# Performance work log

Measured on AMD Instinct MI355X. Metric: run time of the kernel, lower is better.

## Reference

```python
import jax, jax.numpy as jnp
import numpy as np

B = 8192        # number of contexts
T_SIDE = 10     # num_cx_tokens_per_side
NT = 10         # cx_max_num_types
V_TOK = 5000
V_TYP = 5000
D_TOK = 128
D_TYP = 32
H = 32          # hole_rnn_layer_size
D_IN = D_TOK + D_TYP  # 160


def setup_inputs() -> dict:
    key = jax.random.key(0)
    ks = jax.random.split(key, 32)
    def n(k, shape, scale=1.0):
        return jax.random.normal(k, shape, dtype=jnp.float32) * scale
    def rmask(k, shape):
        m = jax.random.randint(k, shape, 0, 2).astype(bool)
        return m.at[:, :, 0].set(True)  # first type slot always valid (as in data loader)
    inp = {}
    inp['tokens_before'] = jax.random.randint(ks[0], (B, T_SIDE), 0, V_TOK, dtype=jnp.int32)
    inp['types_before'] = jax.random.randint(ks[1], (B, T_SIDE, NT), 0, V_TYP, dtype=jnp.int32)
    inp['mask_before'] = rmask(ks[2], (B, T_SIDE, NT))
    inp['tokens_after'] = jax.random.randint(ks[3], (B, T_SIDE), 0, V_TOK, dtype=jnp.int32)
    inp['types_after'] = jax.random.randint(ks[4], (B, T_SIDE, NT), 0, V_TYP, dtype=jnp.int32)
    inp['mask_after'] = rmask(ks[5], (B, T_SIDE, NT))
    inp['token_embeddings'] = n(ks[6], (V_TOK, D_TOK))
    inp['type_embeddings'] = n(ks[7], (V_TYP, D_TYP))
    inp['hole_representation'] = n(ks[8], (1, 1, D_IN))
    # GRU kernels (TF GRUCell layout): gate kernel [(in+h), 2h], candidate [(in+h), h]
    i = 9
    for layer, din in ((0, D_IN), (1, 2 * H)):
        for d in ('fw', 'bw'):
            inp[f'gk_{d}{layer}'] = n(ks[i], (din + H, 2 * H), 0.1); i += 1
            inp[f'gb_{d}{layer}'] = jnp.zeros((2 * H,), jnp.float32)
            inp[f'ck_{d}{layer}'] = n(ks[i], (din + H, H), 0.1); i += 1
            inp[f'cb_{d}{layer}'] = jnp.zeros((H,), jnp.float32)
    return inp


def _embed(tokens, types, mask, tok_emb, typ_emb):
    te = tok_emb[tokens]                                 # [B,T,128]
    ty = typ_emb[types]                                  # [B,T,NT,32]
    ty = ty + (1.0 - mask[..., None].astype(jnp.float32)) * -1000.0
    ty = jnp.max(ty, axis=2)                             # masked max over types -> [B,T,32]
    return jnp.concatenate([te, ty], axis=-1)            # [B,T,160]


def _gru(x_seq, gk, gb, ck, cb):
    # x_seq: [T,B,D]; TF GRUCell math: r,u = sigmoid([x,h]Wg+bg); c = tanh([x, r*h]Wc+bc); h' = u*h+(1-u)*c
    h0 = jnp.zeros((x_seq.shape[1], cb.shape[0]), x_seq.dtype)
    def step(h, x):
        ru = jax.nn.sigmoid(jnp.concatenate([x, h], -1) @ gk + gb)
        r, u = jnp.split(ru, 2, axis=-1)
        c = jnp.tanh(jnp.concatenate([x, r * h], -1) @ ck + cb)
        h_new = u * h + (1.0 - u) * c
        return h_new, h_new
    _, ys = jax.lax.scan(step, h0, x_seq)
    return ys                                            # [T,B,H]


def _bidir(x_seq, pf, pb):
    fw = _gru(x_seq, *pf)
    bw = jnp.flip(_gru(jnp.flip(x_seq, 0), *pb), 0)
    return jnp.concatenate([fw, bw], axis=-1)            # [T,B,2H]


def reference(tokens_before, types_before, mask_before, tokens_after, types_after, mask_after,
              token_embeddings, type_embeddings, hole_representation,
              gk_fw0, gb_fw0, ck_fw0, cb_fw0, gk_bw0, gb_bw0, ck_bw0, cb_bw0,
              gk_fw1, gb_fw1, ck_fw1, cb_fw1, gk_bw1, gb_bw1, ck_bw1, cb_bw1):
    before = _embed(tokens_before, types_before, mask_before, token_embeddings, type_embeddings)
    after = _embed(tokens_after, types_after, mask_after, token_embeddings, type_embeddings)
    nb = before.shape[0]
    hole = jnp.broadcast_to(hole_representation, (nb, 1, D_IN))
    seq = jnp.concatenate([before, hole, after], axis=1)  # [B,21,160]
    x = jnp.transpose(seq, (1, 0, 2))                     # [T,B,D]
    y0 = _bidir(x, (gk_fw0, gb_fw0, ck_fw0, cb_fw0), (gk_bw0, gb_bw0, ck_bw0, cb_bw0))
    y1 = _bidir(y0, (gk_fw1, gb_fw1, ck_fw1, cb_fw1), (gk_bw1, gb_bw1, ck_bw1, cb_bw1))
    return jnp.transpose(y1, (1, 0, 2))                   # [B,21,64]
```

## Files before the change

kernel.cpp:

```cpp
#include <hip/hip_runtime.h>


typedef __attribute__((ext_vector_type(8))) short short8;
typedef __attribute__((ext_vector_type(8))) __bf16 bf16x8;
typedef __attribute__((ext_vector_type(4))) float f32x4;
typedef unsigned short ushort_t;

#define U_TOKEMB  0
#define U_TYPEMB  640000
#define U_HOLE    800000
#define U_GKFW0   800160
#define U_GBFW0   812448
#define U_CKFW0   812512
#define U_CBFW0   818656
#define U_GKBW0   818688
#define U_GBBW0   830976
#define U_CKBW0   831040
#define U_CBBW0   837184
#define U_GKFW1   837216
#define U_GBFW1   843360
#define U_CKFW1   843424
#define U_CBFW1   846496
#define U_GKBW1   846528
#define U_GBBW1   852672
#define U_CKBW1   852736
#define U_CBBW1   855808

#define Y0A_OFF   (4u << 20)
#define TYPF_OFF  (25u << 20)

__device__ __forceinline__ float bf2f(unsigned int u) {
  union { unsigned int i; float f; } v; v.i = u << 16; return v.f;
}
__device__ __forceinline__ unsigned short f2bf(float f) {
  unsigned int u = __float_as_uint(f);
  u += 0x7fffu + ((u >> 16) & 1u);
  return (unsigned short)(u >> 16);
}
__device__ __forceinline__ f32x4 mfma16(short8 a, short8 b, f32x4 c) {
  return __builtin_amdgcn_mfma_f32_16x16x32_bf16(
      __builtin_bit_cast(bf16x8, a), __builtin_bit_cast(bf16x8, b), c, 0, 0, 0);
}
__device__ __forceinline__ float sgm(float x) {
  x = fminf(fmaxf(x, -30.f), 30.f);
  return __fdividef(1.f, 1.f + __expf(-x));
}
__device__ __forceinline__ float tnh(float x) {
  x = fminf(fmaxf(x, -15.f), 15.f);
  float e = __expf(2.f * x);
  return (e - 1.f) * __fdividef(1.f, e + 1.f);
}

__global__ void k0_detect(const ushort_t* __restrict__ probe_f,
                          const unsigned* __restrict__ probe_m,
                          const unsigned* __restrict__ probe_t,
                          int* __restrict__ flags) {
  const int lane = threadIdx.x;
  int cnt = 0;
#pragma unroll
  for (int i = 0; i < 4; ++i) {
    unsigned e = ((unsigned)probe_f[lane + i * 64] >> 7) & 0xffu;
    if (e == 0u || (e >= 112u && e <= 134u)) cnt++;
  }
#pragma unroll
  for (int off = 32; off > 0; off >>= 1) cnt += __shfl_down(cnt, off, 64);
  const unsigned v = probe_m[lane];
  const unsigned long long bytelike =
      __ballot((v > 1u) && (v != 0x3F800000u) && ((v & 0xFEFEFEFEu) == 0u));
  const unsigned tv = probe_t[lane];
  const unsigned long long tlooksTypes =
      __ballot(!(tv == 0u || tv == 1u || tv == 0x3F800000u));
  if (lane == 0) {
    flags[0] = (cnt < 205) ? 1 : 0;
    flags[1] = bytelike ? 1 : 0;
    flags[2] = tlooksTypes ? 0 : 1;
  }
}

struct Cvt19 { const void* src[19]; int len[19]; int dst[19]; };

__global__ void kcvt(Cvt19 a, ushort_t* __restrict__ cvt, const int* __restrict__ flags) {
  const int fp32 = flags[0];
  int gid = blockIdx.x * blockDim.x + threadIdx.x;
#pragma unroll 1
  for (int s = 0; s < 19; ++s) {
    if (gid < a.len[s]) {
      cvt[a.dst[s] + gid] = fp32 ? f2bf(((const float*)a.src[s])[gid])
                                 : ((const ushort_t*)a.src[s])[gid];
      return;
    }
    gid -= a.len[s];
  }
}

__global__ __launch_bounds__(256) void ktypmax(
    const void* __restrict__ slot_tb, const void* __restrict__ slot_mb,
    const void* __restrict__ slot_ta, const void* __restrict__ slot_ma,
    const ushort_t* __restrict__ cvt, uint4* __restrict__ typf,
    const int* __restrict__ flags) {
  const int wv = threadIdx.x >> 6;
  const int lane = threadIdx.x & 63;
  const int q = lane >> 4, nl = lane & 15;
  const int job = blockIdx.x * 4 + wv;
  const int st = job >> 9;
  const int btile = job & 511;
  const int side = (st >= 10) ? 1 : 0;
  const int ts = st - side * 10;
  const int b = btile * 16 + nl;
  const int sw = flags[2];
  const int bytem = flags[1];
  const int* tys = side ? (const int*)(sw ? slot_ma : slot_ta)
                        : (const int*)(sw ? slot_mb : slot_tb);
  const void* msk = side ? (sw ? slot_ta : slot_ma)
                         : (sw ? slot_tb : slot_mb);
  const int base = (b * 10 + ts) * 10;
  float mx[8];
#pragma unroll
  for (int j = 0; j < 8; ++j) mx[j] = -1e30f;
#pragma unroll
  for (int nt = 0; nt < 10; ++nt) {
    const int ty = tys[base + nt];
    const bool mv = bytem ? (((const unsigned char*)msk)[base + nt] != 0)
                          : (((const unsigned*)msk)[base + nt] != 0u);
    const float pen = mv ? 0.f : -1000.f;
    uint4 e = *reinterpret_cast<const uint4*>(cvt + U_TYPEMB + (size_t)ty * 32 + q * 8);
    const unsigned w[4] = {e.x, e.y, e.z, e.w};
#pragma unroll
    for (int j2 = 0; j2 < 4; ++j2) {
      mx[2 * j2]     = fmaxf(mx[2 * j2],     bf2f(w[j2] & 0xffffu) + pen);
      mx[2 * j2 + 1] = fmaxf(mx[2 * j2 + 1], bf2f(w[j2] >> 16) + pen);
    }
  }
  short8 v;
#pragma unroll
  for (int j = 0; j < 8; ++j) v[j] = (short)f2bf(mx[j]);
  typf[(size_t)job * 64 + lane] = __builtin_bit_cast(uint4, v);
}

__device__ __forceinline__ void gatherX(
    int t, int btile, int lane,
    const int* __restrict__ tok_b, const int* __restrict__ tok_a,
    const ushort_t* __restrict__ cvt, const uint4* __restrict__ typf,
    short8 af[5]) {
  const int q = lane >> 4, nl = lane & 15;
  if (t == 10) {
#pragma unroll
    for (int kt = 0; kt < 5; ++kt)
      af[kt] = __builtin_bit_cast(short8,
          *reinterpret_cast<const uint4*>(cvt + U_HOLE + kt * 32 + q * 8));
    return;
  }
  const int ts = (t < 10) ? t : t - 11;
  const int side = (t < 10) ? 0 : 1;
  const int b = btile * 16 + nl;
  const int tok = (side ? tok_a : tok_b)[b * 10 + ts];
#pragma unroll
  for (int kt = 0; kt < 4; ++kt)
    af[kt] = __builtin_bit_cast(short8,
        *reinterpret_cast<const uint4*>(cvt + U_TOKEMB + (size_t)tok * 128 + kt * 32 + q * 8));
  af[4] = __builtin_bit_cast(short8,
      typf[((size_t)(side * 10 + ts) * 512 + btile) * 64 + lane]);
}

__global__ __launch_bounds__(256, 1) void krec0(
    const int* __restrict__ tok_b, const int* __restrict__ tok_a,
    const ushort_t* __restrict__ cvt, const uint4* __restrict__ typf,
    uint4* __restrict__ y0a) {
  __shared__ __align__(16) ushort_t hbuf[4][2][16 * 40];
  const int wv = threadIdx.x >> 6;
  const int lane = threadIdx.x & 63;
  const int q = lane >> 4, nl = lane & 15;
  const int job = blockIdx.x * 4 + wv;
  const int dir = job & 1, btile = job >> 1;

  const ushort_t* gk = cvt + (dir ? U_GKBW0 : U_GKFW0);
  const ushort_t* ck = cvt + (dir ? U_CKBW0 : U_CKFW0);
  const ushort_t* gb = cvt + (dir ? U_GBBW0 : U_GBFW0);
  const ushort_t* cb = cvt + (dir ? U_CBBW0 : U_CBFW0);

  short8 wg[5][4], wc[5][2], wgh[4], wch[2];
#pragma unroll
  for (int kt = 0; kt < 5; ++kt) {
#pragma unroll
    for (int tn = 0; tn < 4; ++tn) {
      short8 v;
#pragma unroll
      for (int j = 0; j < 8; ++j) v[j] = (short)gk[(kt * 32 + q * 8 + j) * 64 + tn * 16 + nl];
      wg[kt][tn] = v;
    }
#pragma unroll
    for (int tn = 0; tn < 2; ++tn) {
      short8 v;
#pragma unroll
      for (int j = 0; j < 8; ++j) v[j] = (short)ck[(kt * 32 + q * 8 + j) * 32 + tn * 16 + nl];
      wc[kt][tn] = v;
    }
  }
#pragma unroll
  for (int tn = 0; tn < 4; ++tn) {
    short8 v;
#pragma unroll
    for (int j = 0; j < 8; ++j) v[j] = (short)gk[(160 + q * 8 + j) * 64 + tn * 16 + nl];
    wgh[tn] = v;
  }
#pragma unroll
  for (int tn = 0; tn < 2; ++tn) {
    short8 v;
#pragma unroll
    for (int j = 0; j < 8; ++j) v[j] = (short)ck[(160 + q * 8 + j) * 32 + tn * 16 + nl];
    wch[tn] = v;
  }
  float gb4[4], cb4[2];
#pragma unroll
  for (int tn = 0; tn < 4; ++tn) gb4[tn] = bf2f((unsigned)gb[tn * 16 + nl]);
#pragma unroll
  for (int tn = 0; tn < 2; ++tn) cb4[tn] = bf2f((unsigned)cb[tn * 16 + nl]);

  f32x4 hc0 = {0.f, 0.f, 0.f, 0.f}, hc1 = {0.f, 0.f, 0.f, 0.f};
  short8 hA = {0, 0, 0, 0, 0, 0, 0, 0};
  ushort_t* hb0 = hbuf[wv][0];
  ushort_t* hb1 = hbuf[wv][1];

  short8 afc[5], afn[5];
  gatherX(dir ? 20 : 0, btile, lane, tok_b, tok_a, cvt, typf, afc);

  for (int s = 0; s < 21; ++s) {
    const int t = dir ? 20 - s : s;
    if (s < 20)
      gatherX(dir ? t - 1 : t + 1, btile, lane, tok_b, tok_a, cvt, typf, afn);

    f32x4 ru[4];
#pragma unroll
    for (int tn = 0; tn < 4; ++tn) {
      f32x4 acc = {gb4[tn], gb4[tn], gb4[tn], gb4[tn]};
#pragma unroll
      for (int kt = 0; kt < 5; ++kt) acc = mfma16(afc[kt], wg[kt][tn], acc);
      acc = mfma16(hA, wgh[tn], acc);
      ru[tn] = acc;
    }
#pragma unroll
    for (int tn = 0; tn < 4; ++tn)
#pragma unroll
      for (int r = 0; r < 4; ++r) ru[tn][r] = sgm(ru[tn][r]);

#pragma unroll
    for (int r = 0; r < 4; ++r) {
      hb0[(q * 4 + r) * 40 + nl]      = f2bf(ru[0][r] * hc0[r]);
      hb0[(q * 4 + r) * 40 + 16 + nl] = f2bf(ru[1][r] * hc1[r]);
    }
    short8 rhA = *reinterpret_cast<const short8*>(hb0 + nl * 40 + q * 8);

    f32x4 cc0 = {cb4[0], cb4[0], cb4[0], cb4[0]};
    f32x4 cc1 = {cb4[1], cb4[1], cb4[1], cb4[1]};
#pragma unroll
    for (int kt = 0; kt < 5; ++kt) {
      cc0 = mfma16(afc[kt], wc[kt][0], cc0);
      cc1 = mfma16(afc[kt], wc[kt][1], cc1);
    }
    cc0 = mfma16(rhA, wch[0], cc0);
    cc1 = mfma16(rhA, wch[1], cc1);
#pragma unroll
    for (int r = 0; r < 4; ++r) {
      const float c0 = tnh(cc0[r]), c1 = tnh(cc1[r]);
      const float u0 = ru[2][r], u1 = ru[3][r];
      hc0[r] = u0 * hc0[r] + (1.f - u0) * c0;
      hc1[r] = u1 * hc1[r] + (1.f - u1) * c1;
    }

#pragma unroll
    for (int r = 0; r < 4; ++r) {
      hb1[(q * 4 + r) * 40 + nl]      = f2bf(hc0[r]);
      hb1[(q * 4 + r) * 40 + 16 + nl] = f2bf(hc1[r]);
    }
    hA = *reinterpret_cast<const short8*>(hb1 + nl * 40 + q * 8);
    y0a[((size_t)(t * 512 + btile) * 2 + dir) * 64 + lane] = __builtin_bit_cast(uint4, hA);

    if (s < 20) {
#pragma unroll
      for (int kt = 0; kt < 5; ++kt) afc[kt] = afn[kt];
    }
  }
}

__global__ __launch_bounds__(256, 1) void k3b(
    const ushort_t* __restrict__ cvt, const uint4* __restrict__ y0a,
    float* __restrict__ out) {
  __shared__ __align__(16) ushort_t hbuf[4][2][16 * 40];
  const int wv = threadIdx.x >> 6;
  const int lane = threadIdx.x & 63;
  const int q = lane >> 4, nl = lane & 15;
  const int job = blockIdx.x * 4 + wv;
  const int dir = job & 1, btile = job >> 1;
  const ushort_t* gk = cvt + (dir ? U_GKBW1 : U_GKFW1);
  const ushort_t* ck = cvt + (dir ? U_CKBW1 : U_CKFW1);
  const ushort_t* gb = cvt + (dir ? U_GBBW1 : U_GBFW1);
  const ushort_t* cb = cvt + (dir ? U_CBBW1 : U_CBFW1);

  short8 wg[3][4], wc[3][2];
#pragma unroll
  for (int kt = 0; kt < 3; ++kt) {
#pragma unroll
    for (int tn = 0; tn < 4; ++tn) {
      short8 v;
#pragma unroll
      for (int j = 0; j < 8; ++j) v[j] = (short)gk[(kt * 32 + q * 8 + j) * 64 + tn * 16 + nl];
      wg[kt][tn] = v;
    }
#pragma unroll
    for (int tn = 0; tn < 2; ++tn) {
      short8 v;
#pragma unroll
      for (int j = 0; j < 8; ++j) v[j] = (short)ck[(kt * 32 + q * 8 + j) * 32 + tn * 16 + nl];
      wc[kt][tn] = v;
    }
  }
  float gb4[4], cb4[2];
#pragma unroll
  for (int tn = 0; tn < 4; ++tn) gb4[tn] = bf2f((unsigned)gb[tn * 16 + nl]);
#pragma unroll
  for (int tn = 0; tn < 2; ++tn) cb4[tn] = bf2f((unsigned)cb[tn * 16 + nl]);

  f32x4 hc0 = {0.f, 0.f, 0.f, 0.f}, hc1 = {0.f, 0.f, 0.f, 0.f};
  short8 hA = {0, 0, 0, 0, 0, 0, 0, 0};
  ushort_t* hb0 = hbuf[wv][0];
  ushort_t* hb1 = hbuf[wv][1];

  short8 ya0, ya1, yn0, yn1;
  {
    const int t0 = dir ? 20 : 0;
    ya0 = __builtin_bit_cast(short8, y0a[((size_t)(t0 * 512 + btile) * 2 + 0) * 64 + lane]);
    ya1 = __builtin_bit_cast(short8, y0a[((size_t)(t0 * 512 + btile) * 2 + 1) * 64 + lane]);
  }

  for (int s = 0; s < 21; ++s) {
    const int t = dir ? 20 - s : s;
    if (s < 20) {
      const int t2 = dir ? t - 1 : t + 1;
      yn0 = __builtin_bit_cast(short8, y0a[((size_t)(t2 * 512 + btile) * 2 + 0) * 64 + lane]);
      yn1 = __builtin_bit_cast(short8, y0a[((size_t)(t2 * 512 + btile) * 2 + 1) * 64 + lane]);
    }

    f32x4 ru[4];
#pragma unroll
    for (int tn = 0; tn < 4; ++tn) {
      f32x4 acc = {gb4[tn], gb4[tn], gb4[tn], gb4[tn]};
      acc = mfma16(ya0, wg[0][tn], acc);
      acc = mfma16(ya1, wg[1][tn], acc);
      acc = mfma16(hA,  wg[2][tn], acc);
      ru[tn] = acc;
    }
#pragma unroll
    for (int tn = 0; tn < 4; ++tn)
#pragma unroll
      for (int r = 0; r < 4; ++r) ru[tn][r] = sgm(ru[tn][r]);

#pragma unroll
    for (int r = 0; r < 4; ++r) {
      hb0[(q * 4 + r) * 40 + nl]      = f2bf(ru[0][r] * hc0[r]);
      hb0[(q * 4 + r) * 40 + 16 + nl] = f2bf(ru[1][r] * hc1[r]);
    }
    short8 rhA = *reinterpret_cast<const short8*>(hb0 + nl * 40 + q * 8);

    f32x4 cc0 = {cb4[0], cb4[0], cb4[0], cb4[0]};
    cc0 = mfma16(ya0, wc[0][0], cc0);
    cc0 = mfma16(ya1, wc[1][0], cc0);
    cc0 = mfma16(rhA, wc[2][0], cc0);
    f32x4 cc1 = {cb4[1], cb4[1], cb4[1], cb4[1]};
    cc1 = mfma16(ya0, wc[0][1], cc1);
    cc1 = mfma16(ya1, wc[1][1], cc1);
    cc1 = mfma16(rhA, wc[2][1], cc1);

#pragma unroll
    for (int r = 0; r < 4; ++r) {
      const float c0 = tnh(cc0[r]), c1 = tnh(cc1[r]);
      const float u0 = ru[2][r], u1 = ru[3][r];
      hc0[r] = u0 * hc0[r] + (1.f - u0) * c0;
      hc1[r] = u1 * hc1[r] + (1.f - u1) * c1;
    }

#pragma unroll
    for (int r = 0; r < 4; ++r) {
      hb1[(q * 4 + r) * 40 + nl]      = f2bf(hc0[r]);
      hb1[(q * 4 + r) * 40 + 16 + nl] = f2bf(hc1[r]);
    }
    hA = *reinterpret_cast<const short8*>(hb1 + nl * 40 + q * 8);

#pragma unroll
    for (int r = 0; r < 4; ++r) {
      const size_t o = ((size_t)(btile * 16 + q * 4 + r) * 21 + t) * 64 + dir * 32 + nl;
      out[o]      = hc0[r];
      out[o + 16] = hc1[r];
    }

    if (s < 20) { ya0 = yn0; ya1 = yn1; }
  }
}

extern "C" void kernel_launch(void* const* d_in, const int* in_sizes, int n_in,
                              void* d_out, int out_size, void* d_ws, size_t ws_size,
                              hipStream_t stream)
{
  const int* tok_b = (const int*)d_in[0];
  const void* slot_tb = d_in[1];
  const void* slot_mb = d_in[2];
  const int* tok_a = (const int*)d_in[3];
  const void* slot_ta = d_in[4];
  const void* slot_ma = d_in[5];

  int* flags = (int*)d_ws;
  ushort_t* cvt = (ushort_t*)((char*)d_ws + 64);
  uint4* y0a = (uint4*)((char*)d_ws + Y0A_OFF);
  uint4* typf = (uint4*)((char*)d_ws + TYPF_OFF);

  k0_detect<<<dim3(1), dim3(64), 0, stream>>>(
      (const ushort_t*)d_in[6], (const unsigned*)slot_mb, (const unsigned*)slot_tb,
      flags);

  static const int slen[19] = {640000, 160000, 160,
                               12288, 64, 6144, 32, 12288, 64, 6144, 32,
                               6144, 64, 3072, 32, 6144, 64, 3072, 32};
  static const int sdst[19] = {U_TOKEMB, U_TYPEMB, U_HOLE,
                               U_GKFW0, U_GBFW0, U_CKFW0, U_CBFW0,
                               U_GKBW0, U_GBBW0, U_CKBW0, U_CBBW0,
                               U_GKFW1, U_GBFW1, U_CKFW1, U_CBFW1,
                               U_GKBW1, U_GBBW1, U_CKBW1, U_CBBW1};
  Cvt19 a;
  int tot = 0;
  for (int i = 0; i < 19; ++i) {
    a.src[i] = d_in[6 + i]; a.len[i] = slen[i]; a.dst[i] = sdst[i]; tot += slen[i];
  }
  kcvt<<<dim3((tot + 255) / 256), dim3(256), 0, stream>>>(a, cvt, flags);

  ktypmax<<<dim3(2560), dim3(256), 0, stream>>>(
      slot_tb, slot_mb, slot_ta, slot_ma, cvt, typf, flags);

  krec0<<<dim3(256), dim3(256), 0, stream>>>(tok_b, tok_a, cvt, typf, y0a);

  k3b<<<dim3(256), dim3(256), 0, stream>>>(cvt, y0a, (float*)d_out);
}
```

Baseline: 212.3 us.

## Hoist input projections out of GRU recurrences into parallel precompute kernels

Splits each GRU layer into a fully parallel input-projection kernel (kxp0/kxp1) that computes x·W plus bias for all timesteps into an fp32 workspace, and a recurrence kernel that only performs the hidden-state MFMAs per step. A small swizzle kernel pre-lays out the weights as MFMA fragments so all kernels load them with one vector load per fragment. The serial recurrence loop gets much shorter and the gather/projection work moves to highly parallel launches, at the cost of writing and reading a large fp32 intermediate per layer and two extra launches.

```diff
diff --git a/kernel.cpp b/kernel.cpp
--- a/kernel.cpp
+++ b/kernel.cpp
@@ -28,6 +28,10 @@
 
 #define Y0A_OFF   (4u << 20)
 #define TYPF_OFF  (25u << 20)
+#define WF_OFF    (37u << 20)
+#define XG_OFF    (40u << 20)
+
+#define XG_TSTRIDE ((size_t)512 * 2 * 6 * 64)
 
 __device__ __forceinline__ float bf2f(unsigned int u) {
   union { unsigned int i; float f; } v; v.i = u << 16; return v.f;
@@ -91,6 +95,37 @@
     }
     gid -= a.len[s];
   }
+}
+
+__global__ void kswz(const ushort_t* __restrict__ cvt, uint4* __restrict__ wf) {
+  const int id = blockIdx.x * blockDim.x + threadIdx.x;
+  if (id >= 108 * 64) return;
+  const int frag = id >> 6, lane = id & 63;
+  const int q = lane >> 4, nl = lane & 15;
+  const int layer = (frag >= 72) ? 1 : 0;
+  const int fr = layer ? frag - 72 : frag;
+  const int nper = layer ? 18 : 36;
+  const int d = fr / nper;
+  const int f = fr - d * nper;
+  const ushort_t* gk = layer ? (cvt + (d ? U_GKBW1 : U_GKFW1))
+                             : (cvt + (d ? U_GKBW0 : U_GKFW0));
+  const ushort_t* ck = layer ? (cvt + (d ? U_CKBW1 : U_CKFW1))
+                             : (cvt + (d ? U_CKBW0 : U_CKFW0));
+  const ushort_t* src; int row0, colw, coloff;
+  if (!layer) {
+    if (f < 20)      { src = gk; row0 = (f >> 2) * 32; colw = 64; coloff = (f & 3) * 16; }
+    else if (f < 30) { int g = f - 20; src = ck; row0 = (g >> 1) * 32; colw = 32; coloff = (g & 1) * 16; }
+    else if (f < 34) { src = gk; row0 = 160; colw = 64; coloff = (f - 30) * 16; }
+    else             { src = ck; row0 = 160; colw = 32; coloff = (f - 34) * 16; }
+  } else {
+    if (f < 12)      { src = gk; row0 = (f >> 2) * 32; colw = 64; coloff = (f & 3) * 16; }
+    else             { int g = f - 12; src = ck; row0 = (g >> 1) * 32; colw = 32; coloff = (g & 1) * 16; }
+  }
+  short8 v;
+#pragma unroll
+  for (int j = 0; j < 8; ++j)
+    v[j] = (short)src[(row0 + q * 8 + j) * colw + coloff + nl];
+  wf[frag * 64 + lane] = __builtin_bit_cast(uint4, v);
 }
 
 __global__ __launch_bounds__(256) void ktypmax(
@@ -162,10 +197,49 @@
       typf[((size_t)(side * 10 + ts) * 512 + btile) * 64 + lane]);
 }
 
-__global__ __launch_bounds__(256, 1) void krec0(
+__global__ __launch_bounds__(256) void kxp0(
     const int* __restrict__ tok_b, const int* __restrict__ tok_a,
     const ushort_t* __restrict__ cvt, const uint4* __restrict__ typf,
-    uint4* __restrict__ y0a) {
+    const uint4* __restrict__ wf, uint4* __restrict__ xg) {
+  const int wv = threadIdx.x >> 6;
+  const int lane = threadIdx.x & 63;
+  const int nl = lane & 15;
+  const int job = blockIdx.x * 4 + wv;
+  const int dir = job & 1;
+  const int r2 = job >> 1;
+  const int t = r2 >> 9, btile = r2 & 511;
+
+  short8 af[5];
+  gatherX(t, btile, lane, tok_b, tok_a, cvt, typf, af);
+
+  const uint4* wfL0 = wf + dir * 36 * 64;
+  const ushort_t* gb = cvt + (dir ? U_GBBW0 : U_GBFW0);
+  const ushort_t* cb = cvt + (dir ? U_CBBW0 : U_CBFW0);
+  uint4* xo = xg + (size_t)job * 6 * 64;
+
+#pragma unroll
+  for (int tn = 0; tn < 4; ++tn) {
+    const float b = bf2f((unsigned)gb[tn * 16 + nl]);
+    f32x4 acc = {b, b, b, b};
+#pragma unroll
+    for (int kt = 0; kt < 5; ++kt)
+      acc = mfma16(af[kt], __builtin_bit_cast(short8, wfL0[(kt * 4 + tn) * 64 + lane]), acc);
+    xo[tn * 64 + lane] = __builtin_bit_cast(uint4, acc);
+  }
+#pragma unroll
+  for (int tn = 0; tn < 2; ++tn) {
+    const float b = bf2f((unsigned)cb[tn * 16 + nl]);
+    f32x4 acc = {b, b, b, b};
+#pragma unroll
+    for (int kt = 0; kt < 5; ++kt)
+      acc = mfma16(af[kt], __builtin_bit_cast(short8, wfL0[(20 + kt * 2 + tn) * 64 + lane]), acc);
+    xo[(4 + tn) * 64 + lane] = __builtin_bit_cast(uint4, acc);
+  }
+}
+
+__global__ __launch_bounds__(256) void krec0(
+    const ushort_t* __restrict__ cvt, const uint4* __restrict__ wf,
+    const uint4* __restrict__ xg, uint4* __restrict__ y0a) {
   __shared__ __align__(16) ushort_t hbuf[4][2][16 * 40];
   const int wv = threadIdx.x >> 6;
   const int lane = threadIdx.x & 63;
@@ -173,71 +247,40 @@
   const int job = blockIdx.x * 4 + wv;
   const int dir = job & 1, btile = job >> 1;
 
-  const ushort_t* gk = cvt + (dir ? U_GKBW0 : U_GKFW0);
-  const ushort_t* ck = cvt + (dir ? U_CKBW0 : U_CKFW0);
-  const ushort_t* gb = cvt + (dir ? U_GBBW0 : U_GBFW0);
-  const ushort_t* cb = cvt + (dir ? U_CBBW0 : U_CBFW0);
-
-  short8 wg[5][4], wc[5][2], wgh[4], wch[2];
-#pragma unroll
-  for (int kt = 0; kt < 5; ++kt) {
-#pragma unroll
-    for (int tn = 0; tn < 4; ++tn) {
-      short8 v;
-#pragma unroll
-      for (int j = 0; j < 8; ++j) v[j] = (short)gk[(kt * 32 + q * 8 + j) * 64 + tn * 16 + nl];
-      wg[kt][tn] = v;
-    }
-#pragma unroll
-    for (int tn = 0; tn < 2; ++tn) {
-      short8 v;
-#pragma unroll
-      for (int j = 0; j < 8; ++j) v[j] = (short)ck[(kt * 32 + q * 8 + j) * 32 + tn * 16 + nl];
-      wc[kt][tn] = v;
-    }
-  }
-#pragma unroll
-  for (int tn = 0; tn < 4; ++tn) {
-    short8 v;
-#pragma unroll
-    for (int j = 0; j < 8; ++j) v[j] = (short)gk[(160 + q * 8 + j) * 64 + tn * 16 + nl];
-    wgh[tn] = v;
-  }
-#pragma unroll
-  for (int tn = 0; tn < 2; ++tn) {
-    short8 v;
-#pragma unroll
-    for (int j = 0; j < 8; ++j) v[j] = (short)ck[(160 + q * 8 + j) * 32 + tn * 16 + nl];
-    wch[tn] = v;
-  }
-  float gb4[4], cb4[2];
-#pragma unroll
-  for (int tn = 0; tn < 4; ++tn) gb4[tn] = bf2f((unsigned)gb[tn * 16 + nl]);
-#pragma unroll
-  for (int tn = 0; tn < 2; ++tn) cb4[tn] = bf2f((unsigned)cb[tn * 16 + nl]);
+  const uint4* wfL0 = wf + dir * 36 * 64;
+  short8 wgh[4], wch[2];
+#pragma unroll
+  for (int tn = 0; tn < 4; ++tn)
+    wgh[tn] = __builtin_bit_cast(short8, wfL0[(30 + tn) * 64 + lane]);
+#pragma unroll
+  for (int tn = 0; tn < 2; ++tn)
+    wch[tn] = __builtin_bit_cast(short8, wfL0[(34 + tn) * 64 + lane]);
 
   f32x4 hc0 = {0.f, 0.f, 0.f, 0.f}, hc1 = {0.f, 0.f, 0.f, 0.f};
   short8 hA = {0, 0, 0, 0, 0, 0, 0, 0};
   ushort_t* hb0 = hbuf[wv][0];
   ushort_t* hb1 = hbuf[wv][1];
 
-  short8 afc[5], afn[5];
-  gatherX(dir ? 20 : 0, btile, lane, tok_b, tok_a, cvt, typf, afc);
+  const int t0 = dir ? 20 : 0;
+  const uint4* xp = xg + ((size_t)(t0 * 512 + btile) * 2 + dir) * 6 * 64 + lane;
+  const long step = dir ? -(long)XG_TSTRIDE : (long)XG_TSTRIDE;
+
+  f32x4 cur[6], nxt[6];
+#pragma unroll
+  for (int tn = 0; tn < 6; ++tn) cur[tn] = __builtin_bit_cast(f32x4, xp[tn * 64]);
 
   for (int s = 0; s < 21; ++s) {
     const int t = dir ? 20 - s : s;
-    if (s < 20)
-      gatherX(dir ? t - 1 : t + 1, btile, lane, tok_b, tok_a, cvt, typf, afn);
+    if (s < 20) {
+      const uint4* xn = xp + step;
+#pragma unroll
+      for (int tn = 0; tn < 6; ++tn) nxt[tn] = __builtin_bit_cast(f32x4, xn[tn * 64]);
+      xp = xn;
+    }
 
     f32x4 ru[4];
 #pragma unroll
-    for (int tn = 0; tn < 4; ++tn) {
-      f32x4 acc = {gb4[tn], gb4[tn], gb4[tn], gb4[tn]};
-#pragma unroll
-      for (int kt = 0; kt < 5; ++kt) acc = mfma16(afc[kt], wg[kt][tn], acc);
-      acc = mfma16(hA, wgh[tn], acc);
-      ru[tn] = acc;
-    }
+    for (int tn = 0; tn < 4; ++tn) ru[tn] = mfma16(hA, wgh[tn], cur[tn]);
 #pragma unroll
     for (int tn = 0; tn < 4; ++tn)
 #pragma unroll
@@ -250,15 +293,8 @@
     }
     short8 rhA = *reinterpret_cast<const short8*>(hb0 + nl * 40 + q * 8);
 
-    f32x4 cc0 = {cb4[0], cb4[0], cb4[0], cb4[0]};
-    f32x4 cc1 = {cb4[1], cb4[1], cb4[1], cb4[1]};
-#pragma unroll
-    for (int kt = 0; kt < 5; ++kt) {
-      cc0 = mfma16(afc[kt], wc[kt][0], cc0);
-      cc1 = mfma16(afc[kt], wc[kt][1], cc1);
-    }
-    cc0 = mfma16(rhA, wch[0], cc0);
-    cc1 = mfma16(rhA, wch[1], cc1);
+    f32x4 cc0 = mfma16(rhA, wch[0], cur[4]);
+    f32x4 cc1 = mfma16(rhA, wch[1], cur[5]);
 #pragma unroll
     for (int r = 0; r < 4; ++r) {
       const float c0 = tnh(cc0[r]), c1 = tnh(cc1[r]);
@@ -277,13 +313,50 @@
 
     if (s < 20) {
 #pragma unroll
-      for (int kt = 0; kt < 5; ++kt) afc[kt] = afn[kt];
-    }
-  }
-}
-
-__global__ __launch_bounds__(256, 1) void k3b(
+      for (int tn = 0; tn < 6; ++tn) cur[tn] = nxt[tn];
+    }
+  }
+}
+
+__global__ __launch_bounds__(256) void kxp1(
     const ushort_t* __restrict__ cvt, const uint4* __restrict__ y0a,
+    const uint4* __restrict__ wf, uint4* __restrict__ xg) {
+  const int wv = threadIdx.x >> 6;
+  const int lane = threadIdx.x & 63;
+  const int nl = lane & 15;
+  const int job = blockIdx.x * 4 + wv;
+  const int dir = job & 1;
+  const int r2 = job >> 1;
+  const int t = r2 >> 9, btile = r2 & 511;
+
+  const short8 ya0 = __builtin_bit_cast(short8, y0a[((size_t)(t * 512 + btile) * 2 + 0) * 64 + lane]);
+  const short8 ya1 = __builtin_bit_cast(short8, y0a[((size_t)(t * 512 + btile) * 2 + 1) * 64 + lane]);
+
+  const uint4* wfL1 = wf + (72 + dir * 18) * 64;
+  const ushort_t* gb = cvt + (dir ? U_GBBW1 : U_GBFW1);
+  const ushort_t* cb = cvt + (dir ? U_CBBW1 : U_CBFW1);
+  uint4* xo = xg + (size_t)job * 6 * 64;
+
+#pragma unroll
+  for (int tn = 0; tn < 4; ++tn) {
+    const float b = bf2f((unsigned)gb[tn * 16 + nl]);
+    f32x4 acc = {b, b, b, b};
+    acc = mfma16(ya0, __builtin_bit_cast(short8, wfL1[tn * 64 + lane]), acc);
+    acc = mfma16(ya1, __builtin_bit_cast(short8, wfL1[(4 + tn) * 64 + lane]), acc);
+    xo[tn * 64 + lane] = __builtin_bit_cast(uint4, acc);
+  }
+#pragma unroll
+  for (int tn = 0; tn < 2; ++tn) {
+    const float b = bf2f((unsigned)cb[tn * 16 + nl]);
+    f32x4 acc = {b, b, b, b};
+    acc = mfma16(ya0, __builtin_bit_cast(short8, wfL1[(12 + tn) * 64 + lane]), acc);
+    acc = mfma16(ya1, __builtin_bit_cast(short8, wfL1[(14 + tn) * 64 + lane]), acc);
+    xo[(4 + tn) * 64 + lane] = __builtin_bit_cast(uint4, acc);
+  }
+}
+
+__global__ __launch_bounds__(256) void k3b(
+    const uint4* __restrict__ wf, const uint4* __restrict__ xg,
     float* __restrict__ out) {
   __shared__ __align__(16) ushort_t hbuf[4][2][16 * 40];
   const int wv = threadIdx.x >> 6;
@@ -291,64 +364,41 @@
   const int q = lane >> 4, nl = lane & 15;
   const int job = blockIdx.x * 4 + wv;
   const int dir = job & 1, btile = job >> 1;
-  const ushort_t* gk = cvt + (dir ? U_GKBW1 : U_GKFW1);
-  const ushort_t* ck = cvt + (dir ? U_CKBW1 : U_CKFW1);
-  const ushort_t* gb = cvt + (dir ? U_GBBW1 : U_GBFW1);
-  const ushort_t* cb = cvt + (dir ? U_CBBW1 : U_CBFW1);
-
-  short8 wg[3][4], wc[3][2];
-#pragma unroll
-  for (int kt = 0; kt < 3; ++kt) {
-#pragma unroll
-    for (int tn = 0; tn < 4; ++tn) {
-      short8 v;
-#pragma unroll
-      for (int j = 0; j < 8; ++j) v[j] = (short)gk[(kt * 32 + q * 8 + j) * 64 + tn * 16 + nl];
-      wg[kt][tn] = v;
-    }
-#pragma unroll
-    for (int tn = 0; tn < 2; ++tn) {
-      short8 v;
-#pragma unroll
-      for (int j = 0; j < 8; ++j) v[j] = (short)ck[(kt * 32 + q * 8 + j) * 32 + tn * 16 + nl];
-      wc[kt][tn] = v;
-    }
-  }
-  float gb4[4], cb4[2];
-#pragma unroll
-  for (int tn = 0; tn < 4; ++tn) gb4[tn] = bf2f((unsigned)gb[tn * 16 + nl]);
-#pragma unroll
-  for (int tn = 0; tn < 2; ++tn) cb4[tn] = bf2f((unsigned)cb[tn * 16 + nl]);
+
+  const uint4* wfL1 = wf + (72 + dir * 18) * 64;
+  short8 wgh[4], wch[2];
+#pragma unroll
+  for (int tn = 0; tn < 4; ++tn)
+    wgh[tn] = __builtin_bit_cast(short8, wfL1[(8 + tn) * 64 + lane]);
+#pragma unroll
+  for (int tn = 0; tn < 2; ++tn)
+    wch[tn] = __builtin_bit_cast(short8, wfL1[(16 + tn) * 64 + lane]);
 
   f32x4 hc0 = {0.f, 0.f, 0.f, 0.f}, hc1 = {0.f, 0.f, 0.f, 0.f};
   short8 hA = {0, 0, 0, 0, 0, 0, 0, 0};
   ushort_t* hb0 = hbuf[wv][0];
   ushort_t* hb1 = hbuf[wv][1];
 
-  short8 ya0, ya1, yn0, yn1;
-  {
-    const int t0 = dir ? 20 : 0;
-    ya0 = __builtin_bit_cast(short8, y0a[((size_t)(t0 * 512 + btile) * 2 + 0) * 64 + lane]);
-    ya1 = __builtin_bit_cast(short8, y0a[((size_t)(t0 * 512 + btile) * 2 + 1) * 64 + lane]);
-  }
+  const int t0 = dir ? 20 : 0;
+  const uint4* xp = xg + ((size_t)(t0 * 512 + btile) * 2 + dir) * 6 * 64 + lane;
+  const long step = dir ? -(long)XG_TSTRIDE : (long)XG_TSTRIDE;
+
+  f32x4 cur[6], nxt[6];
+#pragma unroll
+  for (int tn = 0; tn < 6; ++tn) cur[tn] = __builtin_bit_cast(f32x4, xp[tn * 64]);
 
   for (int s = 0; s < 21; ++s) {
     const int t = dir ? 20 - s : s;
     if (s < 20) {
-      const int t2 = dir ? t - 1 : t + 1;
-      yn0 = __builtin_bit_cast(short8, y0a[((size_t)(t2 * 512 + btile) * 2 + 0) * 64 + lane]);
-      yn1 = __builtin_bit_cast(short8, y0a[((size_t)(t2 * 512 + btile) * 2 + 1) * 64 + lane]);
+      const uint4* xn = xp + step;
+#pragma unroll
+      for (int tn = 0; tn < 6; ++tn) nxt[tn] = __builtin_bit_cast(f32x4, xn[tn * 64]);
+      xp = xn;
     }
 
     f32x4 ru[4];
 #pragma unroll
-    for (int tn = 0; tn < 4; ++tn) {
-      f32x4 acc = {gb4[tn], gb4[tn], gb4[tn], gb4[tn]};
-      acc = mfma16(ya0, wg[0][tn], acc);
-      acc = mfma16(ya1, wg[1][tn], acc);
-      acc = mfma16(hA,  wg[2][tn], acc);
-      ru[tn] = acc;
-    }
+    for (int tn = 0; tn < 4; ++tn) ru[tn] = mfma16(hA, wgh[tn], cur[tn]);
 #pragma unroll
     for (int tn = 0; tn < 4; ++tn)
 #pragma unroll
@@ -361,15 +411,8 @@
     }
     short8 rhA = *reinterpret_cast<const short8*>(hb0 + nl * 40 + q * 8);
 
-    f32x4 cc0 = {cb4[0], cb4[0], cb4[0], cb4[0]};
-    cc0 = mfma16(ya0, wc[0][0], cc0);
-    cc0 = mfma16(ya1, wc[1][0], cc0);
-    cc0 = mfma16(rhA, wc[2][0], cc0);
-    f32x4 cc1 = {cb4[1], cb4[1], cb4[1], cb4[1]};
-    cc1 = mfma16(ya0, wc[0][1], cc1);
-    cc1 = mfma16(ya1, wc[1][1], cc1);
-    cc1 = mfma16(rhA, wc[2][1], cc1);
-
+    f32x4 cc0 = mfma16(rhA, wch[0], cur[4]);
+    f32x4 cc1 = mfma16(rhA, wch[1], cur[5]);
 #pragma unroll
     for (int r = 0; r < 4; ++r) {
       const float c0 = tnh(cc0[r]), c1 = tnh(cc1[r]);
@@ -392,7 +435,10 @@
       out[o + 16] = hc1[r];
     }
 
-    if (s < 20) { ya0 = yn0; ya1 = yn1; }
+    if (s < 20) {
+#pragma unroll
+      for (int tn = 0; tn < 6; ++tn) cur[tn] = nxt[tn];
+    }
   }
 }
 
@@ -411,6 +457,8 @@
   ushort_t* cvt = (ushort_t*)((char*)d_ws + 64);
   uint4* y0a = (uint4*)((char*)d_ws + Y0A_OFF);
   uint4* typf = (uint4*)((char*)d_ws + TYPF_OFF);
+  uint4* wf  = (uint4*)((char*)d_ws + WF_OFF);
+  uint4* xg  = (uint4*)((char*)d_ws + XG_OFF);
 
   k0_detect<<<dim3(1), dim3(64), 0, stream>>>(
       (const ushort_t*)d_in[6], (const unsigned*)slot_mb, (const unsigned*)slot_tb,
@@ -431,10 +479,16 @@
   }
   kcvt<<<dim3((tot + 255) / 256), dim3(256), 0, stream>>>(a, cvt, flags);
 
+  kswz<<<dim3(27), dim3(256), 0, stream>>>(cvt, wf);
+
   ktypmax<<<dim3(2560), dim3(256), 0, stream>>>(
       slot_tb, slot_mb, slot_ta, slot_ma, cvt, typf, flags);
 
-  krec0<<<dim3(256), dim3(256), 0, stream>>>(tok_b, tok_a, cvt, typf, y0a);
-
-  k3b<<<dim3(256), dim3(256), 0, stream>>>(cvt, y0a, (float*)d_out);
-}
+  kxp0<<<dim3(5376), dim3(256), 0, stream>>>(tok_b, tok_a, cvt, typf, wf, xg);
+
+  krec0<<<dim3(256), dim3(256), 0, stream>>>(cvt, wf, xg, y0a);
+
+  kxp1<<<dim3(5376), dim3(256), 0, stream>>>(cvt, y0a, wf, xg);
+
+  k3b<<<dim3(256), dim3(256), 0, stream>>>(wf, xg, (float*)d_out);
+}
```

New measurement: 278.5 us. +31.1%, slower.

## Halve rows per wave, pre-swizzle weight fragments, hoist layer-1 input projections

Applied to the files above, without the earlier changes.

Each wave now handles 8 batch rows instead of 16, with the 16-wide MFMA tile half-filled by duplicated rows. This doubles the grid of both recurrent kernels to 512 blocks, with launch bounds set for 2 blocks per CU, so the latency-bound sequential recurrence gets more parallelism. Weight fragments are pre-swizzled once into MFMA layout by a new small kernel, so each wave loads them as contiguous uint4 reads instead of strided scalar gathers. In layer 1 the input projection for the next timestep is computed ahead of the recurrence step, shortening the dependent chain. The cost is twice the MFMA work per useful row and an extra kernel launch.

```diff
diff --git a/kernel.cpp b/kernel.cpp
--- a/kernel.cpp
+++ b/kernel.cpp
@@ -28,6 +28,7 @@
 
 #define Y0A_OFF   (4u << 20)
 #define TYPF_OFF  (25u << 20)
+#define WF_OFF    (37u << 20)
 
 __device__ __forceinline__ float bf2f(unsigned int u) {
   union { unsigned int i; float f; } v; v.i = u << 16; return v.f;
@@ -91,6 +92,37 @@
     }
     gid -= a.len[s];
   }
+}
+
+__global__ void kswz(const ushort_t* __restrict__ cvt, uint4* __restrict__ wf) {
+  const int id = blockIdx.x * blockDim.x + threadIdx.x;
+  if (id >= 108 * 64) return;
+  const int frag = id >> 6, lane = id & 63;
+  const int q = lane >> 4, nl = lane & 15;
+  const int layer = (frag >= 72) ? 1 : 0;
+  const int fr = layer ? frag - 72 : frag;
+  const int nper = layer ? 18 : 36;
+  const int d = fr / nper;
+  const int f = fr - d * nper;
+  const ushort_t* gk = layer ? (cvt + (d ? U_GKBW1 : U_GKFW1))
+                             : (cvt + (d ? U_GKBW0 : U_GKFW0));
+  const ushort_t* ck = layer ? (cvt + (d ? U_CKBW1 : U_CKFW1))
+                             : (cvt + (d ? U_CKBW0 : U_CKFW0));
+  const ushort_t* src; int row0, colw, coloff;
+  if (!layer) {
+    if (f < 20)      { src = gk; row0 = (f >> 2) * 32; colw = 64; coloff = (f & 3) * 16; }
+    else if (f < 30) { int g = f - 20; src = ck; row0 = (g >> 1) * 32; colw = 32; coloff = (g & 1) * 16; }
+    else if (f < 34) { src = gk; row0 = 160; colw = 64; coloff = (f - 30) * 16; }
+    else             { src = ck; row0 = 160; colw = 32; coloff = (f - 34) * 16; }
+  } else {
+    if (f < 12)      { src = gk; row0 = (f >> 2) * 32; colw = 64; coloff = (f & 3) * 16; }
+    else             { int g = f - 12; src = ck; row0 = (g >> 1) * 32; colw = 32; coloff = (g & 1) * 16; }
+  }
+  short8 v;
+#pragma unroll
+  for (int j = 0; j < 8; ++j)
+    v[j] = (short)src[(row0 + q * 8 + j) * colw + coloff + nl];
+  wf[frag * 64 + lane] = __builtin_bit_cast(uint4, v);
 }
 
 __global__ __launch_bounds__(256) void ktypmax(
@@ -137,12 +169,11 @@
   typf[(size_t)job * 64 + lane] = __builtin_bit_cast(uint4, v);
 }
 
-__device__ __forceinline__ void gatherX(
-    int t, int btile, int lane,
+__device__ __forceinline__ void gatherX8(
+    int t, int Rc, int q,
     const int* __restrict__ tok_b, const int* __restrict__ tok_a,
     const ushort_t* __restrict__ cvt, const uint4* __restrict__ typf,
     short8 af[5]) {
-  const int q = lane >> 4, nl = lane & 15;
   if (t == 10) {
 #pragma unroll
     for (int kt = 0; kt < 5; ++kt)
@@ -152,64 +183,48 @@
   }
   const int ts = (t < 10) ? t : t - 11;
   const int side = (t < 10) ? 0 : 1;
-  const int b = btile * 16 + nl;
-  const int tok = (side ? tok_a : tok_b)[b * 10 + ts];
+  const int tok = (side ? tok_a : tok_b)[Rc * 10 + ts];
 #pragma unroll
   for (int kt = 0; kt < 4; ++kt)
     af[kt] = __builtin_bit_cast(short8,
         *reinterpret_cast<const uint4*>(cvt + U_TOKEMB + (size_t)tok * 128 + kt * 32 + q * 8));
   af[4] = __builtin_bit_cast(short8,
-      typf[((size_t)(side * 10 + ts) * 512 + btile) * 64 + lane]);
-}
-
-__global__ __launch_bounds__(256, 1) void krec0(
+      typf[((size_t)(side * 10 + ts) * 512 + (Rc >> 4)) * 64 + q * 16 + (Rc & 15)]);
+}
+
+__global__ __launch_bounds__(256, 2) void krec0(
     const int* __restrict__ tok_b, const int* __restrict__ tok_a,
-    const ushort_t* __restrict__ cvt, const uint4* __restrict__ typf,
-    uint4* __restrict__ y0a) {
+    const ushort_t* __restrict__ cvt, const uint4* __restrict__ wf,
+    const uint4* __restrict__ typf, uint4* __restrict__ y0a) {
   __shared__ __align__(16) ushort_t hbuf[4][2][16 * 40];
   const int wv = threadIdx.x >> 6;
   const int lane = threadIdx.x & 63;
   const int q = lane >> 4, nl = lane & 15;
   const int job = blockIdx.x * 4 + wv;
-  const int dir = job & 1, btile = job >> 1;
-
-  const ushort_t* gk = cvt + (dir ? U_GKBW0 : U_GKFW0);
-  const ushort_t* ck = cvt + (dir ? U_CKBW0 : U_CKFW0);
+  const int dir = job & 1, jb = job >> 1;
+  const int R = jb * 8 + nl;
+  const int Rc = (R < 8191) ? R : 8191;
+
+  const uint4* wfL0 = wf + dir * 36 * 64;
+  short8 wg[5][4], wc[5][2], wgh[4], wch[2];
+#pragma unroll
+  for (int kt = 0; kt < 5; ++kt) {
+#pragma unroll
+    for (int tn = 0; tn < 4; ++tn)
+      wg[kt][tn] = __builtin_bit_cast(short8, wfL0[(kt * 4 + tn) * 64 + lane]);
+#pragma unroll
+    for (int tn = 0; tn < 2; ++tn)
+      wc[kt][tn] = __builtin_bit_cast(short8, wfL0[(20 + kt * 2 + tn) * 64 + lane]);
+  }
+#pragma unroll
+  for (int tn = 0; tn < 4; ++tn)
+    wgh[tn] = __builtin_bit_cast(short8, wfL0[(30 + tn) * 64 + lane]);
+#pragma unroll
+  for (int tn = 0; tn < 2; ++tn)
+    wch[tn] = __builtin_bit_cast(short8, wfL0[(34 + tn) * 64 + lane]);
+
   const ushort_t* gb = cvt + (dir ? U_GBBW0 : U_GBFW0);
   const ushort_t* cb = cvt + (dir ? U_CBBW0 : U_CBFW0);
-
-  short8 wg[5][4], wc[5][2], wgh[4], wch[2];
-#pragma unroll
-  for (int kt = 0; kt < 5; ++kt) {
-#pragma unroll
-    for (int tn = 0; tn < 4; ++tn) {
-      short8 v;
-#pragma unroll
-      for (int j = 0; j < 8; ++j) v[j] = (short)gk[(kt * 32 + q * 8 + j) * 64 + tn * 16 + nl];
-      wg[kt][tn] = v;
-    }
-#pragma unroll
-    for (int tn = 0; tn < 2; ++tn) {
-      short8 v;
-#pragma unroll
-      for (int j = 0; j < 8; ++j) v[j] = (short)ck[(kt * 32 + q * 8 + j) * 32 + tn * 16 + nl];
-      wc[kt][tn] = v;
-    }
-  }
-#pragma unroll
-  for (int tn = 0; tn < 4; ++tn) {
-    short8 v;
-#pragma unroll
-    for (int j = 0; j < 8; ++j) v[j] = (short)gk[(160 + q * 8 + j) * 64 + tn * 16 + nl];
-    wgh[tn] = v;
-  }
-#pragma unroll
-  for (int tn = 0; tn < 2; ++tn) {
-    short8 v;
-#pragma unroll
-    for (int j = 0; j < 8; ++j) v[j] = (short)ck[(160 + q * 8 + j) * 32 + tn * 16 + nl];
-    wch[tn] = v;
-  }
   float gb4[4], cb4[2];
 #pragma unroll
   for (int tn = 0; tn < 4; ++tn) gb4[tn] = bf2f((unsigned)gb[tn * 16 + nl]);
@@ -221,13 +236,16 @@
   ushort_t* hb0 = hbuf[wv][0];
   ushort_t* hb1 = hbuf[wv][1];
 
+  const int stile = jb >> 1;
+  const int sslot = nl + 8 * (jb & 1);
+
   short8 afc[5], afn[5];
-  gatherX(dir ? 20 : 0, btile, lane, tok_b, tok_a, cvt, typf, afc);
+  gatherX8(dir ? 20 : 0, Rc, q, tok_b, tok_a, cvt, typf, afc);
 
   for (int s = 0; s < 21; ++s) {
     const int t = dir ? 20 - s : s;
     if (s < 20)
-      gatherX(dir ? t - 1 : t + 1, btile, lane, tok_b, tok_a, cvt, typf, afn);
+      gatherX8(dir ? t - 1 : t + 1, Rc, q, tok_b, tok_a, cvt, typf, afn);
 
     f32x4 ru[4];
 #pragma unroll
@@ -273,7 +291,9 @@
       hb1[(q * 4 + r) * 40 + 16 + nl] = f2bf(hc1[r]);
     }
     hA = *reinterpret_cast<const short8*>(hb1 + nl * 40 + q * 8);
-    y0a[((size_t)(t * 512 + btile) * 2 + dir) * 64 + lane] = __builtin_bit_cast(uint4, hA);
+    if (nl < 8)
+      y0a[((size_t)(t * 512 + stile) * 2 + dir) * 64 + q * 16 + sslot] =
+          __builtin_bit_cast(uint4, hA);
 
     if (s < 20) {
 #pragma unroll
@@ -282,38 +302,35 @@
   }
 }
 
-__global__ __launch_bounds__(256, 1) void k3b(
-    const ushort_t* __restrict__ cvt, const uint4* __restrict__ y0a,
-    float* __restrict__ out) {
+__global__ __launch_bounds__(256, 2) void k3b(
+    const ushort_t* __restrict__ cvt, const uint4* __restrict__ wf,
+    const uint4* __restrict__ y0a, float* __restrict__ out) {
   __shared__ __align__(16) ushort_t hbuf[4][2][16 * 40];
   const int wv = threadIdx.x >> 6;
   const int lane = threadIdx.x & 63;
   const int q = lane >> 4, nl = lane & 15;
   const int job = blockIdx.x * 4 + wv;
-  const int dir = job & 1, btile = job >> 1;
-  const ushort_t* gk = cvt + (dir ? U_GKBW1 : U_GKFW1);
-  const ushort_t* ck = cvt + (dir ? U_CKBW1 : U_CKFW1);
+  const int dir = job & 1, jb = job >> 1;
+  const int R = jb * 8 + nl;
+  const int Rc = (R < 8191) ? R : 8191;
+  const int rt = Rc >> 4, rs = Rc & 15;
+
+  const uint4* wfL1 = wf + (72 + dir * 18) * 64;
+  short8 wgx0[4], wgx1[4], wgh[4], wcx0[2], wcx1[2], wch[2];
+#pragma unroll
+  for (int tn = 0; tn < 4; ++tn) {
+    wgx0[tn] = __builtin_bit_cast(short8, wfL1[tn * 64 + lane]);
+    wgx1[tn] = __builtin_bit_cast(short8, wfL1[(4 + tn) * 64 + lane]);
+    wgh[tn]  = __builtin_bit_cast(short8, wfL1[(8 + tn) * 64 + lane]);
+  }
+#pragma unroll
+  for (int tn = 0; tn < 2; ++tn) {
+    wcx0[tn] = __builtin_bit_cast(short8, wfL1[(12 + tn) * 64 + lane]);
+    wcx1[tn] = __builtin_bit_cast(short8, wfL1[(14 + tn) * 64 + lane]);
+    wch[tn]  = __builtin_bit_cast(short8, wfL1[(16 + tn) * 64 + lane]);
+  }
   const ushort_t* gb = cvt + (dir ? U_GBBW1 : U_GBFW1);
   const ushort_t* cb = cvt + (dir ? U_CBBW1 : U_CBFW1);
-
-  short8 wg[3][4], wc[3][2];
-#pragma unroll
-  for (int kt = 0; kt < 3; ++kt) {
-#pragma unroll
-    for (int tn = 0; tn < 4; ++tn) {
-      short8 v;
-#pragma unroll
-      for (int j = 0; j < 8; ++j) v[j] = (short)gk[(kt * 32 + q * 8 + j) * 64 + tn * 16 + nl];
-      wg[kt][tn] = v;
-    }
-#pragma unroll
-    for (int tn = 0; tn < 2; ++tn) {
-      short8 v;
-#pragma unroll
-      for (int j = 0; j < 8; ++j) v[j] = (short)ck[(kt * 32 + q * 8 + j) * 32 + tn * 16 + nl];
-      wc[kt][tn] = v;
-    }
-  }
   float gb4[4], cb4[2];
 #pragma unroll
   for (int tn = 0; tn < 4; ++tn) gb4[tn] = bf2f((unsigned)gb[tn * 16 + nl]);
@@ -325,30 +342,44 @@
   ushort_t* hb0 = hbuf[wv][0];
   ushort_t* hb1 = hbuf[wv][1];
 
-  short8 ya0, ya1, yn0, yn1;
+#define LOAD_YA(tt, d0, d1)                                                      \
+  do {                                                                           \
+    d0 = __builtin_bit_cast(short8,                                              \
+        y0a[((size_t)((tt) * 512 + rt) * 2 + 0) * 64 + q * 16 + rs]);            \
+    d1 = __builtin_bit_cast(short8,                                              \
+        y0a[((size_t)((tt) * 512 + rt) * 2 + 1) * 64 + q * 16 + rs]);            \
+  } while (0)
+
+  f32x4 px[6];
   {
     const int t0 = dir ? 20 : 0;
-    ya0 = __builtin_bit_cast(short8, y0a[((size_t)(t0 * 512 + btile) * 2 + 0) * 64 + lane]);
-    ya1 = __builtin_bit_cast(short8, y0a[((size_t)(t0 * 512 + btile) * 2 + 1) * 64 + lane]);
+    short8 ya0, ya1;
+    LOAD_YA(t0, ya0, ya1);
+#pragma unroll
+    for (int tn = 0; tn < 4; ++tn) {
+      f32x4 acc = {gb4[tn], gb4[tn], gb4[tn], gb4[tn]};
+      acc = mfma16(ya0, wgx0[tn], acc);
+      acc = mfma16(ya1, wgx1[tn], acc);
+      px[tn] = acc;
+    }
+#pragma unroll
+    for (int tn = 0; tn < 2; ++tn) {
+      f32x4 acc = {cb4[tn], cb4[tn], cb4[tn], cb4[tn]};
+      acc = mfma16(ya0, wcx0[tn], acc);
+      acc = mfma16(ya1, wcx1[tn], acc);
+      px[4 + tn] = acc;
+    }
   }
 
   for (int s = 0; s < 21; ++s) {
     const int t = dir ? 20 - s : s;
-    if (s < 20) {
-      const int t2 = dir ? t - 1 : t + 1;
-      yn0 = __builtin_bit_cast(short8, y0a[((size_t)(t2 * 512 + btile) * 2 + 0) * 64 + lane]);
-      yn1 = __builtin_bit_cast(short8, y0a[((size_t)(t2 * 512 + btile) * 2 + 1) * 64 + lane]);
-    }
+
+    short8 yn0, yn1;
+    if (s < 20) LOAD_YA(dir ? t - 1 : t + 1, yn0, yn1);
 
     f32x4 ru[4];
 #pragma unroll
-    for (int tn = 0; tn < 4; ++tn) {
-      f32x4 acc = {gb4[tn], gb4[tn], gb4[tn], gb4[tn]};
-      acc = mfma16(ya0, wg[0][tn], acc);
-      acc = mfma16(ya1, wg[1][tn], acc);
-      acc = mfma16(hA,  wg[2][tn], acc);
-      ru[tn] = acc;
-    }
+    for (int tn = 0; tn < 4; ++tn) ru[tn] = mfma16(hA, wgh[tn], px[tn]);
 #pragma unroll
     for (int tn = 0; tn < 4; ++tn)
 #pragma unroll
@@ -361,15 +392,8 @@
     }
     short8 rhA = *reinterpret_cast<const short8*>(hb0 + nl * 40 + q * 8);
 
-    f32x4 cc0 = {cb4[0], cb4[0], cb4[0], cb4[0]};
-    cc0 = mfma16(ya0, wc[0][0], cc0);
-    cc0 = mfma16(ya1, wc[1][0], cc0);
-    cc0 = mfma16(rhA, wc[2][0], cc0);
-    f32x4 cc1 = {cb4[1], cb4[1], cb4[1], cb4[1]};
-    cc1 = mfma16(ya0, wc[0][1], cc1);
-    cc1 = mfma16(ya1, wc[1][1], cc1);
-    cc1 = mfma16(rhA, wc[2][1], cc1);
-
+    f32x4 cc0 = mfma16(rhA, wch[0], px[4]);
+    f32x4 cc1 = mfma16(rhA, wch[1], px[5]);
 #pragma unroll
     for (int r = 0; r < 4; ++r) {
       const float c0 = tnh(cc0[r]), c1 = tnh(cc1[r]);
@@ -385,15 +409,33 @@
     }
     hA = *reinterpret_cast<const short8*>(hb1 + nl * 40 + q * 8);
 
-#pragma unroll
-    for (int r = 0; r < 4; ++r) {
-      const size_t o = ((size_t)(btile * 16 + q * 4 + r) * 21 + t) * 64 + dir * 32 + nl;
-      out[o]      = hc0[r];
-      out[o + 16] = hc1[r];
-    }
-
-    if (s < 20) { ya0 = yn0; ya1 = yn1; }
-  }
+    if (q < 2) {
+#pragma unroll
+      for (int r = 0; r < 4; ++r) {
+        const size_t o = ((size_t)(jb * 8 + q * 4 + r) * 21 + t) * 64 + dir * 32 + nl;
+        out[o]      = hc0[r];
+        out[o + 16] = hc1[r];
+      }
+    }
+
+    if (s < 20) {
+#pragma unroll
+      for (int tn = 0; tn < 4; ++tn) {
+        f32x4 acc = {gb4[tn], gb4[tn], gb4[tn], gb4[tn]};
+        acc = mfma16(yn0, wgx0[tn], acc);
+        acc = mfma16(yn1, wgx1[tn], acc);
+        px[tn] = acc;
+      }
+#pragma unroll
+      for (int tn = 0; tn < 2; ++tn) {
+        f32x4 acc = {cb4[tn], cb4[tn], cb4[tn], cb4[tn]};
+        acc = mfma16(yn0, wcx0[tn], acc);
+        acc = mfma16(yn1, wcx1[tn], acc);
+        px[4 + tn] = acc;
+      }
+    }
+  }
+#undef LOAD_YA
 }
 
 extern "C" void kernel_launch(void* const* d_in, const int* in_sizes, int n_in,
@@ -411,6 +453,7 @@
   ushort_t* cvt = (ushort_t*)((char*)d_ws + 64);
   uint4* y0a = (uint4*)((char*)d_ws + Y0A_OFF);
   uint4* typf = (uint4*)((char*)d_ws + TYPF_OFF);
+  uint4* wf  = (uint4*)((char*)d_ws + WF_OFF);
 
   k0_detect<<<dim3(1), dim3(64), 0, stream>>>(
       (const ushort_t*)d_in[6], (const unsigned*)slot_mb, (const unsigned*)slot_tb,
@@ -431,10 +474,12 @@
   }
   kcvt<<<dim3((tot + 255) / 256), dim3(256), 0, stream>>>(a, cvt, flags);
 
+  kswz<<<dim3(27), dim3(256), 0, stream>>>(cvt, wf);
+
   ktypmax<<<dim3(2560), dim3(256), 0, stream>>>(
       slot_tb, slot_mb, slot_ta, slot_ma, cvt, typf, flags);
 
-  krec0<<<dim3(256), dim3(256), 0, stream>>>(tok_b, tok_a, cvt, typf, y0a);
-
-  k3b<<<dim3(256), dim3(256), 0, stream>>>(cvt, y0a, (float*)d_out);
-}
+  krec0<<<dim3(512), dim3(256), 0, stream>>>(tok_b, tok_a, cvt, wf, typf, y0a);
+
+  k3b<<<dim3(512), dim3(256), 0, stream>>>(cvt, wf, y0a, (float*)d_out);
+}
```

Measured after the change: 261.6 us. 23.2% more time.
